# Optimization experiments

Hardware: AMD Instinct MI355X
Metric: run time of the kernel (lower is better)

Reference implementation:

```python
import jax, jax.numpy as jnp
import numpy as np

B, S, H, NH = 2, 2048, 1024, 16
DK = H // NH


def setup_inputs() -> dict:
    key = jax.random.key(0)
    ks = jax.random.split(key, 11)
    sc = 1.0 / np.sqrt(H)
    return {
        "q": jax.random.normal(ks[0], (B, S, H), jnp.float32),
        "v": jax.random.normal(ks[1], (B, S, H), jnp.float32),
        "k": jax.random.normal(ks[2], (B, S, H), jnp.float32),
        "Wq": jax.random.normal(ks[3], (H, H), jnp.float32) * sc,
        "bq": jax.random.normal(ks[4], (H,), jnp.float32) * 0.01,
        "Wk": jax.random.normal(ks[5], (H, H), jnp.float32) * sc,
        "bk": jax.random.normal(ks[6], (H,), jnp.float32) * 0.01,
        "Wv": jax.random.normal(ks[7], (H, H), jnp.float32) * sc,
        "bv": jax.random.normal(ks[8], (H,), jnp.float32) * 0.01,
        "Wo": jax.random.normal(ks[9], (H, H), jnp.float32) * sc,
        "bo": jax.random.normal(ks[10], (H,), jnp.float32) * 0.01,
    }


def reference(q, v, k, Wq, bq, Wk, bk, Wv, bv, Wo, bo):
    b, s, h = q.shape
    # projections; torch Linear computes x @ W.T + b
    qh = (q @ Wq.T + bq).reshape(b, s, NH, DK).transpose(0, 2, 1, 3)  # [B,NH,S,DK]
    kh = (k @ Wk.T + bk).reshape(b, s, NH, DK).transpose(0, 2, 1, 3)
    vh = (v @ Wv.T + bv).reshape(b, s, NH, DK).transpose(0, 2, 1, 3)
    scores = jnp.einsum("bhqd,bhkd->bhqk", qh, kh) / jnp.sqrt(
        jnp.asarray(DK, qh.dtype))  # [B,NH,S,S]
    probs = jax.nn.softmax(scores, axis=-1)
    ctx = jnp.einsum("bhqk,bhkd->bhqd", probs, vh)  # [B,NH,S,DK]
    concat = ctx.transpose(0, 2, 1, 3).reshape(b, s, h)
    return concat @ Wo.T + bo
```

## Files before the change

### kernel.cpp

```cpp
#include <hip/hip_runtime.h>
#include <cstddef>
#include <cstdint>

typedef _Float16 f16x8 __attribute__((ext_vector_type(8)));
typedef _Float16 f16x4 __attribute__((ext_vector_type(4)));
typedef __fp16   h16x2 __attribute__((ext_vector_type(2)));
typedef float    f32x4 __attribute__((ext_vector_type(4)));

constexpr int B_  = 2;
constexpr int S_  = 2048;
constexpr int H_  = 1024;
constexpr int NH_ = 16;
constexpr int DK_ = 64;
constexpr int M_  = B_ * S_;
constexpr int K_  = H_;

constexpr float SOFF = 4.0f;

#define MFMA32(a, b, c) __builtin_amdgcn_mfma_f32_16x16x32_f16((a), (b), (c), 0, 0, 0)
#define MFMA16(a, b, c) __builtin_amdgcn_mfma_f32_16x16x16f16((a), (b), (c), 0, 0, 0)

__device__ __forceinline__ void glds16(const void* g, void* l) {
    __builtin_amdgcn_global_load_lds(
        (const __attribute__((address_space(1))) void*)g,
        (__attribute__((address_space(3))) void*)l, 16, 0, 0);
}

__device__ __forceinline__ void pk2(f16x4& dst, int half, float a, float b) {
    const h16x2 r = __builtin_amdgcn_cvt_pkrtz(a, b);
    reinterpret_cast<h16x2*>(&dst)[half] = r;
}

struct CvtArgs {
    const float* s[7];
    _Float16*    d[7];
    int          n[7];
};

__global__ __launch_bounds__(256) void cvt7(CvtArgs a)
{
    const int seg = blockIdx.y;
    const int i = (blockIdx.x * 256 + threadIdx.x) * 8;
    if (i + 8 <= a.n[seg]) {
        const float4 v0 = *reinterpret_cast<const float4*>(a.s[seg] + i);
        const float4 v1 = *reinterpret_cast<const float4*>(a.s[seg] + i + 4);
        f16x8 o;
        o[0] = (_Float16)v0.x; o[1] = (_Float16)v0.y;
        o[2] = (_Float16)v0.z; o[3] = (_Float16)v0.w;
        o[4] = (_Float16)v1.x; o[5] = (_Float16)v1.y;
        o[6] = (_Float16)v1.z; o[7] = (_Float16)v1.w;
        *reinterpret_cast<f16x8*>(a.d[seg] + i) = o;
    }
}

struct QkvArgs {
    const _Float16* A[3];
    const _Float16* W[3];
    const float*    bias[3];
    _Float16* dstQ;
    _Float16* dstK;
    _Float16* dstV;
    float qscale;
};

__global__ __launch_bounds__(256) void gemm_qkv(QkvArgs args)
{
    constexpr int BM = 128, BN = 128, BK = 32;
    __shared__ __align__(16) _Float16 sm[8192];
    auto As = reinterpret_cast<_Float16(*)[BK]>(sm);
    auto Ws = reinterpret_cast<_Float16(*)[BK]>(sm + 4096);
    auto Tr = reinterpret_cast<_Float16(*)[64]>(sm);

    const int z = blockIdx.z;
    const _Float16* __restrict__ A = args.A[z];
    const _Float16* __restrict__ W = args.W[z];
    const float* __restrict__ bias = args.bias[z];

    const int t = threadIdx.x;
    const int w = t >> 6, lane = t & 63, quad = lane >> 4, l16 = lane & 15;
    const int m0 = blockIdx.y * BM;
    const int n0 = blockIdx.x * BN;
    const int wr = (w & 1) * 64, wc = (w >> 1) * 64;
    const int srow = lane >> 2, scol = (lane & 3) * 8;

    f32x4 acc[4][4];
#pragma unroll
    for (int i = 0; i < 4; ++i)
#pragma unroll
        for (int j = 0; j < 4; ++j) acc[i][j] = (f32x4){0.f, 0.f, 0.f, 0.f};

    for (int k0 = 0; k0 < K_; k0 += BK) {
        glds16(&A[(size_t)(m0 + w * 32 + srow) * K_ + k0 + scol], &As[w * 32][0]);
        glds16(&A[(size_t)(m0 + w * 32 + 16 + srow) * K_ + k0 + scol], &As[w * 32 + 16][0]);
        glds16(&W[(size_t)(n0 + w * 32 + srow) * K_ + k0 + scol], &Ws[w * 32][0]);
        glds16(&W[(size_t)(n0 + w * 32 + 16 + srow) * K_ + k0 + scol], &Ws[w * 32 + 16][0]);
        __syncthreads();

        f16x8 af[4], bf[4];
#pragma unroll
        for (int i = 0; i < 4; ++i)
            af[i] = *reinterpret_cast<const f16x8*>(&As[wr + i * 16 + l16][quad * 8]);
#pragma unroll
        for (int j = 0; j < 4; ++j)
            bf[j] = *reinterpret_cast<const f16x8*>(&Ws[wc + j * 16 + l16][quad * 8]);
#pragma unroll
        for (int i = 0; i < 4; ++i)
#pragma unroll
            for (int j = 0; j < 4; ++j)
                acc[i][j] = MFMA32(af[i], bf[j], acc[i][j]);
        __syncthreads();
    }

    const float scale = (z == 0) ? args.qscale : 1.0f;
    float bv[4];
#pragma unroll
    for (int j = 0; j < 4; ++j) bv[j] = bias[n0 + wc + j * 16 + l16];

    if (z == 2) {
#pragma unroll
        for (int i = 0; i < 4; ++i) {
            const int sb = m0 + wr + i * 16 + quad * 4;
            const int b = sb >> 11, s = sb & (S_ - 1);
#pragma unroll
            for (int j = 0; j < 4; ++j) {
                const int d = wc + j * 16 + l16;
                const int h = blockIdx.x * 2 + (d >> 6);
                const int dd = d & 63;
                const int kt = s >> 4, dt = dd >> 4;
                f16x4 ov;
#pragma unroll
                for (int r = 0; r < 4; ++r) ov[r] = (_Float16)(acc[i][j][r] + bv[j]);
                _Float16* base = args.dstV +
                    ((((size_t)b * NH_ + h) * 128 + kt) * 4 + dt) * 256;
                *reinterpret_cast<f16x4*>(&base[lane * 4]) = ov;
            }
        }
        return;
    }

    _Float16* dst = (z == 0) ? args.dstQ : args.dstK;
    const int b = m0 >> 11, s0 = m0 & (S_ - 1);
#pragma unroll
    for (int ch = 0; ch < 2; ++ch) {
        __syncthreads();
        if ((w >> 1) == ch) {
#pragma unroll
            for (int i = 0; i < 4; ++i)
#pragma unroll
                for (int j = 0; j < 4; ++j)
#pragma unroll
                    for (int r = 0; r < 4; ++r)
                        Tr[wr + i * 16 + quad * 4 + r][j * 16 + l16] =
                            (_Float16)((acc[i][j][r] + bv[j]) * scale);
        }
        __syncthreads();
        const int h = blockIdx.x * 2 + ch;
        _Float16* dbase = dst + ((size_t)(b * NH_ + h) * S_ + s0) * DK_;
#pragma unroll
        for (int p = 0; p < 4; ++p) {
            const int c = t + p * 256;
            *reinterpret_cast<f16x8*>(&dbase[c * 8]) =
                *reinterpret_cast<const f16x8*>(&Tr[c >> 3][(c & 7) * 8]);
        }
    }
}

__global__ __launch_bounds__(256) void gemm_out(
    const _Float16* __restrict__ A, const _Float16* __restrict__ W,
    const float* __restrict__ bias, float* __restrict__ out)
{
    constexpr int BM = 128, BN = 128, BK = 32;
    __shared__ _Float16 As[BM][BK];
    __shared__ _Float16 Ws[BN][BK];

    const int t = threadIdx.x;
    const int w = t >> 6, lane = t & 63, quad = lane >> 4, l16 = lane & 15;
    const int m0 = blockIdx.y * BM;
    const int n0 = blockIdx.x * BN;
    const int wr = (w & 1) * 64, wc = (w >> 1) * 64;
    const int srow = lane >> 2, scol = (lane & 3) * 8;

    f32x4 acc[4][4];
#pragma unroll
    for (int i = 0; i < 4; ++i)
#pragma unroll
        for (int j = 0; j < 4; ++j) acc[i][j] = (f32x4){0.f, 0.f, 0.f, 0.f};

    for (int k0 = 0; k0 < K_; k0 += BK) {
        glds16(&A[(size_t)(m0 + w * 32 + srow) * K_ + k0 + scol], &As[w * 32][0]);
        glds16(&A[(size_t)(m0 + w * 32 + 16 + srow) * K_ + k0 + scol], &As[w * 32 + 16][0]);
        glds16(&W[(size_t)(n0 + w * 32 + srow) * K_ + k0 + scol], &Ws[w * 32][0]);
        glds16(&W[(size_t)(n0 + w * 32 + 16 + srow) * K_ + k0 + scol], &Ws[w * 32 + 16][0]);
        __syncthreads();

        f16x8 af[4], bf[4];
#pragma unroll
        for (int i = 0; i < 4; ++i)
            af[i] = *reinterpret_cast<const f16x8*>(&As[wr + i * 16 + l16][quad * 8]);
#pragma unroll
        for (int j = 0; j < 4; ++j)
            bf[j] = *reinterpret_cast<const f16x8*>(&Ws[wc + j * 16 + l16][quad * 8]);
#pragma unroll
        for (int i = 0; i < 4; ++i)
#pragma unroll
            for (int j = 0; j < 4; ++j)
                acc[i][j] = MFMA32(af[i], bf[j], acc[i][j]);
        __syncthreads();
    }

    float bv[4];
#pragma unroll
    for (int j = 0; j < 4; ++j) bv[j] = bias[n0 + wc + j * 16 + l16];

#pragma unroll
    for (int i = 0; i < 4; ++i)
#pragma unroll
        for (int j = 0; j < 4; ++j)
#pragma unroll
            for (int r = 0; r < 4; ++r)
                out[(size_t)(m0 + wr + i * 16 + quad * 4 + r) * H_ +
                    n0 + wc + j * 16 + l16] = acc[i][j][r] + bv[j];
}

__global__ __launch_bounds__(256) void attn_mfma(
    const _Float16* __restrict__ qh, const _Float16* __restrict__ kh,
    const _Float16* __restrict__ vfrag, _Float16* __restrict__ ctx)
{
    __shared__ float Ob[4][64][36];
    __shared__ float Ls[4][64];
    __shared__ float Linv[64];

    const int t = threadIdx.x;
    const int w = t >> 6, lane = t & 63, quad = lane >> 4, l16 = lane & 15;
    const int q0 = blockIdx.x * 64;
    const int bh = blockIdx.y;

    const _Float16* qb = qh + (size_t)bh * S_ * DK_;
    const _Float16* kb = kh + (size_t)bh * S_ * DK_;
    const _Float16* vb = vfrag + (size_t)bh * 128 * 4 * 256;

    f16x8 qf[4][2];
#pragma unroll
    for (int qt = 0; qt < 4; ++qt)
#pragma unroll
        for (int h2 = 0; h2 < 2; ++h2)
            qf[qt][h2] = *reinterpret_cast<const f16x8*>(
                &qb[(size_t)(q0 + qt * 16 + l16) * DK_ + h2 * 32 + quad * 8]);

    f32x4 o[4][4];
#pragma unroll
    for (int dt = 0; dt < 4; ++dt)
#pragma unroll
        for (int qt = 0; qt < 4; ++qt) o[dt][qt] = (f32x4){0.f, 0.f, 0.f, 0.f};
    float lp_[4];
#pragma unroll
    for (int qt = 0; qt < 4; ++qt) lp_[qt] = 0.f;

    const _Float16* kptr = kb + (size_t)(w * 16 + l16) * DK_ + quad * 8;
    const _Float16* vptr = vb + (size_t)w * 4 * 256 + lane * 4;

    f16x8 kf0 = *reinterpret_cast<const f16x8*>(kptr);
    f16x8 kf1 = *reinterpret_cast<const f16x8*>(kptr + 32);

    for (int ti = 0; ti < 32; ++ti) {
        f16x4 vf[4];
#pragma unroll
        for (int dt = 0; dt < 4; ++dt)
            vf[dt] = *reinterpret_cast<const f16x4*>(vptr + dt * 256);
        vptr += 4 * 4 * 256;

        const _Float16* nkp = (ti < 31) ? kptr + 64 * DK_ : kptr;
        const f16x8 nk0 = *reinterpret_cast<const f16x8*>(nkp);
        const f16x8 nk1 = *reinterpret_cast<const f16x8*>(nkp + 32);
        kptr = nkp;

        f32x4 sc[4];
#pragma unroll
        for (int qt = 0; qt < 4; ++qt) {
            sc[qt] = (f32x4){-SOFF, -SOFF, -SOFF, -SOFF};
            sc[qt] = MFMA32(kf0, qf[qt][0], sc[qt]);
            sc[qt] = MFMA32(kf1, qf[qt][1], sc[qt]);
        }

        f16x4 pf[4];
#pragma unroll
        for (int qt = 0; qt < 4; ++qt) {
            const float p0 = __builtin_amdgcn_exp2f(sc[qt][0]);
            const float p1 = __builtin_amdgcn_exp2f(sc[qt][1]);
            const float p2 = __builtin_amdgcn_exp2f(sc[qt][2]);
            const float p3 = __builtin_amdgcn_exp2f(sc[qt][3]);
            lp_[qt] += (p0 + p1) + (p2 + p3);
            f16x4 pv;
            pk2(pv, 0, p0, p1);
            pk2(pv, 1, p2, p3);
            pf[qt] = pv;
        }

#pragma unroll
        for (int dt = 0; dt < 4; ++dt)
#pragma unroll
            for (int qt = 0; qt < 4; ++qt)
                o[dt][qt] = MFMA16(vf[dt], pf[qt], o[dt][qt]);

        kf0 = nk0;
        kf1 = nk1;
    }

#pragma unroll
    for (int qt = 0; qt < 4; ++qt) {
        float l = lp_[qt];
        l += __shfl_xor(l, 16);
        l += __shfl_xor(l, 32);
        if (quad == 0) Ls[w][qt * 16 + l16] = l;
    }
    __syncthreads();
    if (t < 64)
        Linv[t] = 1.f / (((Ls[0][t] + Ls[1][t]) + (Ls[2][t] + Ls[3][t])));

    const int b = bh >> 4, hh = bh & 15;
    const int dg = t & 3, qq = t >> 2;
#pragma unroll
    for (int ph = 0; ph < 2; ++ph) {
        __syncthreads();
#pragma unroll
        for (int dl = 0; dl < 2; ++dl) {
            const int dt = ph * 2 + dl;
#pragma unroll
            for (int qt = 0; qt < 4; ++qt)
                *reinterpret_cast<f32x4*>(
                    &Ob[w][qt * 16 + l16][dl * 16 + quad * 4]) = o[dt][qt];
        }
        __syncthreads();
        f32x4 s0 = (f32x4){0.f, 0.f, 0.f, 0.f};
        f32x4 s1 = (f32x4){0.f, 0.f, 0.f, 0.f};
#pragma unroll
        for (int ww = 0; ww < 4; ++ww) {
            s0 += *reinterpret_cast<const f32x4*>(&Ob[ww][qq][dg * 8]);
            s1 += *reinterpret_cast<const f32x4*>(&Ob[ww][qq][dg * 8 + 4]);
        }
        const float li = Linv[qq];
        f16x8 ov;
#pragma unroll
        for (int r = 0; r < 4; ++r) {
            ov[r]     = (_Float16)(s0[r] * li);
            ov[4 + r] = (_Float16)(s1[r] * li);
        }
        *reinterpret_cast<f16x8*>(
            &ctx[((size_t)b * S_ + q0 + qq) * H_ + hh * 64 + ph * 32 + dg * 8]) = ov;
    }
}

extern "C" void kernel_launch(void* const* d_in, const int* in_sizes, int n_in,
                              void* d_out, int out_size, void* d_ws,
                              size_t ws_size, hipStream_t stream)
{
    (void)in_sizes; (void)n_in; (void)out_size; (void)ws_size;
    const float* q  = (const float*)d_in[0];
    const float* v  = (const float*)d_in[1];
    const float* k  = (const float*)d_in[2];
    const float* Wq = (const float*)d_in[3];
    const float* bq = (const float*)d_in[4];
    const float* Wk = (const float*)d_in[5];
    const float* bk = (const float*)d_in[6];
    const float* Wv = (const float*)d_in[7];
    const float* bv = (const float*)d_in[8];
    const float* Wo = (const float*)d_in[9];
    const float* bo = (const float*)d_in[10];
    float* out = (float*)d_out;

    constexpr size_t NACT = (size_t)M_ * K_;
    constexpr size_t NW   = (size_t)H_ * H_;
    _Float16* p = (_Float16*)d_ws;
    _Float16* q16  = p;
    _Float16* k16  = p + NACT;
    _Float16* v16  = p + 2 * NACT;
    _Float16* w16q = p + 3 * NACT;
    _Float16* w16k = w16q + NW;
    _Float16* w16v = w16k + NW;
    _Float16* w16o = w16v + NW;
    _Float16* qhd  = w16o + NW;
    _Float16* khd  = qhd + NACT;
    _Float16* vfr  = khd + NACT;
    _Float16* ctx  = q16;

    CvtArgs ca;
    ca.s[0] = q;  ca.d[0] = q16;  ca.n[0] = (int)NACT;
    ca.s[1] = v;  ca.d[1] = v16;  ca.n[1] = (int)NACT;
    ca.s[2] = k;  ca.d[2] = k16;  ca.n[2] = (int)NACT;
    ca.s[3] = Wq; ca.d[3] = w16q; ca.n[3] = (int)NW;
    ca.s[4] = Wk; ca.d[4] = w16k; ca.n[4] = (int)NW;
    ca.s[5] = Wv; ca.d[5] = w16v; ca.n[5] = (int)NW;
    ca.s[6] = Wo; ca.d[6] = w16o; ca.n[6] = (int)NW;
    cvt7<<<dim3(2048, 7), 256, 0, stream>>>(ca);

    QkvArgs ga;
    ga.A[0] = q16;  ga.W[0] = w16q; ga.bias[0] = bq;
    ga.A[1] = k16;  ga.W[1] = w16k; ga.bias[1] = bk;
    ga.A[2] = v16;  ga.W[2] = w16v; ga.bias[2] = bv;
    ga.dstQ = qhd;  ga.dstK = khd;  ga.dstV = vfr;
    ga.qscale = 0.125f * 1.4426950408889634f;

    gemm_qkv<<<dim3(H_ / 128, M_ / 128, 3), 256, 0, stream>>>(ga);

    attn_mfma<<<dim3(S_ / 64, B_ * NH_), 256, 0, stream>>>(qhd, khd, vfr, ctx);

    gemm_out<<<dim3(H_ / 128, M_ / 128), 256, 0, stream>>>(ctx, w16o, bo, out);
}
```

Before: 236.6 us.

## Halve attention and output GEMM tile rows to raise grid size, add MFMA priority hints

The attention kernel now handles 32 queries per block instead of 64, doubling the grid. That block also uses s_setprio around its MFMA groups and packed f32x2 partial row sums. The output GEMM tile drops from 128x128 to 64x128, with each wave covering all 64 rows and 32 columns. The aim is more blocks and waves in flight on the many CUs of MI355X, to improve occupancy and latency hiding. The cost is that K/V data is reloaded twice as often across blocks, and each MFMA tile gets less reuse.

```diff
diff --git a/kernel.cpp b/kernel.cpp
--- a/kernel.cpp
+++ b/kernel.cpp
@@ -6,6 +6,7 @@
 typedef _Float16 f16x4 __attribute__((ext_vector_type(4)));
 typedef __fp16   h16x2 __attribute__((ext_vector_type(2)));
 typedef float    f32x4 __attribute__((ext_vector_type(4)));
+typedef float    f32x2 __attribute__((ext_vector_type(2)));
 
 constexpr int B_  = 2;
 constexpr int S_  = 2048;
@@ -169,7 +170,7 @@
     const _Float16* __restrict__ A, const _Float16* __restrict__ W,
     const float* __restrict__ bias, float* __restrict__ out)
 {
-    constexpr int BM = 128, BN = 128, BK = 32;
+    constexpr int BM = 64, BN = 128, BK = 32;
     __shared__ _Float16 As[BM][BK];
     __shared__ _Float16 Ws[BN][BK];
 
@@ -177,84 +178,85 @@
     const int w = t >> 6, lane = t & 63, quad = lane >> 4, l16 = lane & 15;
     const int m0 = blockIdx.y * BM;
     const int n0 = blockIdx.x * BN;
-    const int wr = (w & 1) * 64, wc = (w >> 1) * 64;
+    const int wc = w * 32;
     const int srow = lane >> 2, scol = (lane & 3) * 8;
 
-    f32x4 acc[4][4];
+    f32x4 acc[4][2];
 #pragma unroll
     for (int i = 0; i < 4; ++i)
 #pragma unroll
-        for (int j = 0; j < 4; ++j) acc[i][j] = (f32x4){0.f, 0.f, 0.f, 0.f};
+        for (int j = 0; j < 2; ++j) acc[i][j] = (f32x4){0.f, 0.f, 0.f, 0.f};
 
     for (int k0 = 0; k0 < K_; k0 += BK) {
-        glds16(&A[(size_t)(m0 + w * 32 + srow) * K_ + k0 + scol], &As[w * 32][0]);
-        glds16(&A[(size_t)(m0 + w * 32 + 16 + srow) * K_ + k0 + scol], &As[w * 32 + 16][0]);
+        glds16(&A[(size_t)(m0 + w * 16 + srow) * K_ + k0 + scol], &As[w * 16][0]);
         glds16(&W[(size_t)(n0 + w * 32 + srow) * K_ + k0 + scol], &Ws[w * 32][0]);
         glds16(&W[(size_t)(n0 + w * 32 + 16 + srow) * K_ + k0 + scol], &Ws[w * 32 + 16][0]);
         __syncthreads();
 
-        f16x8 af[4], bf[4];
+        f16x8 af[4], bf[2];
 #pragma unroll
         for (int i = 0; i < 4; ++i)
-            af[i] = *reinterpret_cast<const f16x8*>(&As[wr + i * 16 + l16][quad * 8]);
-#pragma unroll
-        for (int j = 0; j < 4; ++j)
+            af[i] = *reinterpret_cast<const f16x8*>(&As[i * 16 + l16][quad * 8]);
+#pragma unroll
+        for (int j = 0; j < 2; ++j)
             bf[j] = *reinterpret_cast<const f16x8*>(&Ws[wc + j * 16 + l16][quad * 8]);
 #pragma unroll
         for (int i = 0; i < 4; ++i)
 #pragma unroll
-            for (int j = 0; j < 4; ++j)
+            for (int j = 0; j < 2; ++j)
                 acc[i][j] = MFMA32(af[i], bf[j], acc[i][j]);
         __syncthreads();
     }
 
-    float bv[4];
-#pragma unroll
-    for (int j = 0; j < 4; ++j) bv[j] = bias[n0 + wc + j * 16 + l16];
+    float bvv[2];
+#pragma unroll
+    for (int j = 0; j < 2; ++j) bvv[j] = bias[n0 + wc + j * 16 + l16];
 
 #pragma unroll
     for (int i = 0; i < 4; ++i)
 #pragma unroll
-        for (int j = 0; j < 4; ++j)
+        for (int j = 0; j < 2; ++j)
 #pragma unroll
             for (int r = 0; r < 4; ++r)
-                out[(size_t)(m0 + wr + i * 16 + quad * 4 + r) * H_ +
-                    n0 + wc + j * 16 + l16] = acc[i][j][r] + bv[j];
+                out[(size_t)(m0 + i * 16 + quad * 4 + r) * H_ +
+                    n0 + wc + j * 16 + l16] = acc[i][j][r] + bvv[j];
 }
 
 __global__ __launch_bounds__(256) void attn_mfma(
     const _Float16* __restrict__ qh, const _Float16* __restrict__ kh,
     const _Float16* __restrict__ vfrag, _Float16* __restrict__ ctx)
 {
-    __shared__ float Ob[4][64][36];
-    __shared__ float Ls[4][64];
-    __shared__ float Linv[64];
+    __shared__ float Ob[4][32][36];
+    __shared__ float Ls[4][32];
+    __shared__ float Linv[32];
 
     const int t = threadIdx.x;
     const int w = t >> 6, lane = t & 63, quad = lane >> 4, l16 = lane & 15;
-    const int q0 = blockIdx.x * 64;
+    const int q0 = blockIdx.x * 32;
     const int bh = blockIdx.y;
 
     const _Float16* qb = qh + (size_t)bh * S_ * DK_;
     const _Float16* kb = kh + (size_t)bh * S_ * DK_;
     const _Float16* vb = vfrag + (size_t)bh * 128 * 4 * 256;
 
-    f16x8 qf[4][2];
-#pragma unroll
-    for (int qt = 0; qt < 4; ++qt)
+    f16x8 qf[2][2];
+#pragma unroll
+    for (int qt = 0; qt < 2; ++qt)
 #pragma unroll
         for (int h2 = 0; h2 < 2; ++h2)
             qf[qt][h2] = *reinterpret_cast<const f16x8*>(
                 &qb[(size_t)(q0 + qt * 16 + l16) * DK_ + h2 * 32 + quad * 8]);
 
-    f32x4 o[4][4];
+    const f32x4 msoff = (f32x4){-SOFF, -SOFF, -SOFF, -SOFF};
+
+    f32x4 o[4][2];
 #pragma unroll
     for (int dt = 0; dt < 4; ++dt)
 #pragma unroll
-        for (int qt = 0; qt < 4; ++qt) o[dt][qt] = (f32x4){0.f, 0.f, 0.f, 0.f};
-    float lp_[4];
-#pragma unroll
-    for (int qt = 0; qt < 4; ++qt) lp_[qt] = 0.f;
+        for (int qt = 0; qt < 2; ++qt) o[dt][qt] = (f32x4){0.f, 0.f, 0.f, 0.f};
+    f32x2 lp2[2];
+#pragma unroll
+    for (int qt = 0; qt < 2; ++qt) lp2[qt] = (f32x2){0.f, 0.f};
 
     const _Float16* kptr = kb + (size_t)(w * 16 + l16) * DK_ + quad * 8;
     const _Float16* vptr = vb + (size_t)w * 4 * 256 + lane * 4;
@@ -274,51 +276,56 @@
         const f16x8 nk1 = *reinterpret_cast<const f16x8*>(nkp + 32);
         kptr = nkp;
 
-        f32x4 sc[4];
-#pragma unroll
-        for (int qt = 0; qt < 4; ++qt) {
-            sc[qt] = (f32x4){-SOFF, -SOFF, -SOFF, -SOFF};
-            sc[qt] = MFMA32(kf0, qf[qt][0], sc[qt]);
-            sc[qt] = MFMA32(kf1, qf[qt][1], sc[qt]);
-        }
-
-        f16x4 pf[4];
-#pragma unroll
-        for (int qt = 0; qt < 4; ++qt) {
+        f32x4 sc[2];
+        __builtin_amdgcn_s_setprio(1);
+#pragma unroll
+        for (int qt = 0; qt < 2; ++qt) {
+            f32x4 s0 = MFMA32(kf0, qf[qt][0], msoff);
+            sc[qt] = MFMA32(kf1, qf[qt][1], s0);
+        }
+        __builtin_amdgcn_s_setprio(0);
+
+        f16x4 pf[2];
+#pragma unroll
+        for (int qt = 0; qt < 2; ++qt) {
             const float p0 = __builtin_amdgcn_exp2f(sc[qt][0]);
             const float p1 = __builtin_amdgcn_exp2f(sc[qt][1]);
             const float p2 = __builtin_amdgcn_exp2f(sc[qt][2]);
             const float p3 = __builtin_amdgcn_exp2f(sc[qt][3]);
-            lp_[qt] += (p0 + p1) + (p2 + p3);
+            const f32x2 pa = (f32x2){p0, p1};
+            const f32x2 pb = (f32x2){p2, p3};
+            lp2[qt] += pa + pb;
             f16x4 pv;
             pk2(pv, 0, p0, p1);
             pk2(pv, 1, p2, p3);
             pf[qt] = pv;
         }
 
+        __builtin_amdgcn_s_setprio(1);
 #pragma unroll
         for (int dt = 0; dt < 4; ++dt)
 #pragma unroll
-            for (int qt = 0; qt < 4; ++qt)
+            for (int qt = 0; qt < 2; ++qt)
                 o[dt][qt] = MFMA16(vf[dt], pf[qt], o[dt][qt]);
+        __builtin_amdgcn_s_setprio(0);
 
         kf0 = nk0;
         kf1 = nk1;
     }
 
 #pragma unroll
-    for (int qt = 0; qt < 4; ++qt) {
-        float l = lp_[qt];
+    for (int qt = 0; qt < 2; ++qt) {
+        float l = lp2[qt][0] + lp2[qt][1];
         l += __shfl_xor(l, 16);
         l += __shfl_xor(l, 32);
         if (quad == 0) Ls[w][qt * 16 + l16] = l;
     }
     __syncthreads();
-    if (t < 64)
+    if (t < 32)
         Linv[t] = 1.f / (((Ls[0][t] + Ls[1][t]) + (Ls[2][t] + Ls[3][t])));
 
     const int b = bh >> 4, hh = bh & 15;
-    const int dg = t & 3, qq = t >> 2;
+    const int qq = t >> 3, dgg = t & 7;
 #pragma unroll
     for (int ph = 0; ph < 2; ++ph) {
         __syncthreads();
@@ -326,27 +333,21 @@
         for (int dl = 0; dl < 2; ++dl) {
             const int dt = ph * 2 + dl;
 #pragma unroll
-            for (int qt = 0; qt < 4; ++qt)
+            for (int qt = 0; qt < 2; ++qt)
                 *reinterpret_cast<f32x4*>(
                     &Ob[w][qt * 16 + l16][dl * 16 + quad * 4]) = o[dt][qt];
         }
         __syncthreads();
-        f32x4 s0 = (f32x4){0.f, 0.f, 0.f, 0.f};
-        f32x4 s1 = (f32x4){0.f, 0.f, 0.f, 0.f};
-#pragma unroll
-        for (int ww = 0; ww < 4; ++ww) {
-            s0 += *reinterpret_cast<const f32x4*>(&Ob[ww][qq][dg * 8]);
-            s1 += *reinterpret_cast<const f32x4*>(&Ob[ww][qq][dg * 8 + 4]);
-        }
+        f32x4 s = (f32x4){0.f, 0.f, 0.f, 0.f};
+#pragma unroll
+        for (int ww = 0; ww < 4; ++ww)
+            s += *reinterpret_cast<const f32x4*>(&Ob[ww][qq][dgg * 4]);
         const float li = Linv[qq];
-        f16x8 ov;
-#pragma unroll
-        for (int r = 0; r < 4; ++r) {
-            ov[r]     = (_Float16)(s0[r] * li);
-            ov[4 + r] = (_Float16)(s1[r] * li);
-        }
-        *reinterpret_cast<f16x8*>(
-            &ctx[((size_t)b * S_ + q0 + qq) * H_ + hh * 64 + ph * 32 + dg * 8]) = ov;
+        f16x4 ov;
+#pragma unroll
+        for (int r = 0; r < 4; ++r) ov[r] = (_Float16)(s[r] * li);
+        *reinterpret_cast<f16x4*>(
+            &ctx[((size_t)b * S_ + q0 + qq) * H_ + hh * 64 + ph * 32 + dgg * 4]) = ov;
     }
 }
 
@@ -402,7 +403,7 @@
 
     gemm_qkv<<<dim3(H_ / 128, M_ / 128, 3), 256, 0, stream>>>(ga);
 
-    attn_mfma<<<dim3(S_ / 64, B_ * NH_), 256, 0, stream>>>(qhd, khd, vfr, ctx);
-
-    gemm_out<<<dim3(H_ / 128, M_ / 128), 256, 0, stream>>>(ctx, w16o, bo, out);
-}
+    attn_mfma<<<dim3(S_ / 32, B_ * NH_), 256, 0, stream>>>(qhd, khd, vfr, ctx);
+
+    gemm_out<<<dim3(H_ / 128, M_ / 64), 256, 0, stream>>>(ctx, w16o, bo, out);
+}
```

Result: slower. 263.0 us (+11.1%).
